# Kernel optimization log

Measured on AMD Instinct MI355X. Metric: run time of the kernel, lower is better.

The kernel has to match this reference:

```python
import jax, jax.numpy as jnp
import numpy as np

OUT_H, OUT_W = 7, 7
SPATIAL_SCALE = 0.0625


def setup_inputs() -> dict:
    key = jax.random.key(0)
    kf, kb, kx, ky, kw, kh = jax.random.split(key, 6)
    B, C, H, W = 2, 256, 38, 38
    n_rois = 64
    features = jax.random.normal(kf, (B, C, H, W), dtype=jnp.float32)
    bidx = jax.random.randint(kb, (n_rois,), 0, B)
    x1 = jax.random.randint(kx, (n_rois,), 0, 300)
    y1 = jax.random.randint(ky, (n_rois,), 0, 300)
    x2 = x1 + jax.random.randint(kw, (n_rois,), 32, 300)  # x2 < 600
    y2 = y1 + jax.random.randint(kh, (n_rois,), 32, 300)
    rois = jnp.stack([bidx, x1, y1, x2, y2], axis=1).astype(jnp.int32)
    return {"features": features, "rois": rois}


def _roi_max_pool(features, rois):
    # features: [B,C,H,W]; rois: [N,5] int (batch_idx,x1,y1,x2,y2) in image coords
    B, C, H, W = features.shape
    ridx = rois[:, 0]
    start_w = rois[:, 1].astype(jnp.float32) * SPATIAL_SCALE
    start_h = rois[:, 2].astype(jnp.float32) * SPATIAL_SCALE
    end_w = rois[:, 3].astype(jnp.float32) * SPATIAL_SCALE
    end_h = rois[:, 4].astype(jnp.float32) * SPATIAL_SCALE
    bin_h = jnp.maximum(end_h - start_h, 1.0) / OUT_H  # [N]
    bin_w = jnp.maximum(end_w - start_w, 1.0) / OUT_W

    oh = jnp.arange(OUT_H, dtype=jnp.float32)
    ow = jnp.arange(OUT_W, dtype=jnp.float32)
    # per-roi per-bin [start,end) extents, clipped to feature map (matches floor/ceil+clamp)
    hs = jnp.clip(jnp.floor(oh[None, :] * bin_h[:, None] + start_h[:, None]).astype(jnp.int32), 0, H)
    he = jnp.clip(jnp.ceil((oh[None, :] + 1.0) * bin_h[:, None] + start_h[:, None]).astype(jnp.int32), 0, H)
    ws = jnp.clip(jnp.floor(ow[None, :] * bin_w[:, None] + start_w[:, None]).astype(jnp.int32), 0, W)
    we = jnp.clip(jnp.ceil((ow[None, :] + 1.0) * bin_w[:, None] + start_w[:, None]).astype(jnp.int32), 0, W)

    hgrid = jnp.arange(H)
    wgrid = jnp.arange(W)
    mask_h = (hgrid[None, None, :] >= hs[:, :, None]) & (hgrid[None, None, :] < he[:, :, None])  # [N,oh,H]
    mask_w = (wgrid[None, None, :] >= ws[:, :, None]) & (wgrid[None, None, :] < we[:, :, None])  # [N,ow,W]

    feat = features[ridx]  # [N,C,H,W] gather per roi
    neg = jnp.float32(-jnp.inf)
    # separable masked max: first over W -> [N,C,H,ow]
    t = jnp.where(mask_w[:, None, None, :, :], feat[:, :, :, None, :], neg).max(axis=-1)
    # then over H -> [N,C,oh,ow]
    out = jnp.where(mask_h[:, None, :, :, None], t[:, :, None, :, :], neg).max(axis=3)
    # empty bins (h_end<=h_start or w_end<=w_start) stay zero in the original
    valid = mask_h.any(-1)[:, None, :, None] & mask_w.any(-1)[:, None, None, :]  # [N,1,oh,ow]
    return jnp.where(valid, out, jnp.float32(0.0))


def reference(features, rois):
    return _roi_max_pool(features, rois)
```

## Files before the change

kernel.cpp:

```cpp
#include <hip/hip_runtime.h>

#define OUT_HW 7
#define NCH    256
#define FH     38
#define FW     38


__global__ __launch_bounds__(256) void roi_pool_kernel(
    const float* __restrict__ feat,
    const int*   __restrict__ rois,
    float*       __restrict__ out,
    int total)
{
    int idx = blockIdx.x * blockDim.x + threadIdx.x;
    if (idx >= total) return;

    int ow = idx % OUT_HW;
    int oh = (idx / OUT_HW) % OUT_HW;
    int c  = (idx / (OUT_HW * OUT_HW)) % NCH;
    int r  = idx / (OUT_HW * OUT_HW * NCH);

    const int* roi = rois + r * 5;
    int ridx = roi[0];

    float sw = (float)roi[1] * 0.0625f;
    float sh = (float)roi[2] * 0.0625f;
    float ew = (float)roi[3] * 0.0625f;
    float eh = (float)roi[4] * 0.0625f;

    const float C7 = __uint_as_float(0x3E124925u);
    float bw = __fmul_rn(fmaxf(ew - sw, 1.0f), C7);
    float bh = __fmul_rn(fmaxf(eh - sh, 1.0f), C7);

    int hs = (int)floorf(fmaf((float)oh,       bh, sh));
    int he = (int)ceilf (fmaf((float)(oh + 1), bh, sh));
    int ws = (int)floorf(fmaf((float)ow,       bw, sw));
    int we = (int)ceilf (fmaf((float)(ow + 1), bw, sw));

    hs = min(max(hs, 0), FH);
    he = min(max(he, 0), FH);
    ws = min(max(ws, 0), FW);
    we = min(max(we, 0), FW);

    float m = 0.0f;
    if (hs < he && ws < we) {
        m = -INFINITY;
        const float* base = feat + ((size_t)ridx * NCH + c) * (FH * FW);
        for (int h = hs; h < he; ++h) {
            const float* row = base + h * FW;
            for (int w = ws; w < we; ++w) {
                m = fmaxf(m, row[w]);
            }
        }
    }
    out[idx] = m;
}

extern "C" void kernel_launch(void* const* d_in, const int* in_sizes, int n_in,
                              void* d_out, int out_size, void* d_ws, size_t ws_size,
                              hipStream_t stream) {
    const float* feat = (const float*)d_in[0];
    const int*   rois = (const int*)d_in[1];
    float*       out  = (float*)d_out;

    int total  = out_size;
    int blocks = (total + 255) / 256;
    roi_pool_kernel<<<blocks, 256, 0, stream>>>(feat, rois, out, total);
}
```

Measured before the change: 64.45 us.

## Stage each ROI channel plane in LDS with one wavefront per plane

Each wavefront now loads one whole 38x38 feature plane for its (roi, channel) pair into shared memory with coalesced float4 loads. Its first 49 lanes then compute the 7x7 bin maxima from LDS instead of issuing scattered global reads. This replaces many uncoalesced, partly redundant global loads with one contiguous plane copy, at the cost of loading the full plane even when the ROI covers only part of it. It also adds 23 KB of LDS per block and a block barrier.

```diff
diff --git a/kernel.cpp b/kernel.cpp
--- a/kernel.cpp
+++ b/kernel.cpp
@@ -4,24 +4,40 @@
 #define NCH    256
 #define FH     38
 #define FW     38
+#define PLANE  (FH * FW)
+#define PLANE4 (PLANE / 4)
+#define PLANE_PAD4 364
 
 
 __global__ __launch_bounds__(256) void roi_pool_kernel(
     const float* __restrict__ feat,
     const int*   __restrict__ rois,
-    float*       __restrict__ out,
-    int total)
+    float*       __restrict__ out)
 {
-    int idx = blockIdx.x * blockDim.x + threadIdx.x;
-    if (idx >= total) return;
+    __shared__ float4 lds4[4][PLANE_PAD4];
 
-    int ow = idx % OUT_HW;
-    int oh = (idx / OUT_HW) % OUT_HW;
-    int c  = (idx / (OUT_HW * OUT_HW)) % NCH;
-    int r  = idx / (OUT_HW * OUT_HW * NCH);
+    int tid  = threadIdx.x;
+    int wv   = tid >> 6;
+    int lane = tid & 63;
+    int p    = blockIdx.x * 4 + wv;
+    int c    = p & (NCH - 1);
+    int r    = p >> 8;
 
     const int* roi = rois + r * 5;
     int ridx = roi[0];
+
+    const float4* src4 = (const float4*)(feat + ((size_t)ridx * NCH + c) * PLANE);
+    float4* dst4 = &lds4[wv][0];
+    #pragma unroll
+    for (int i = 0; i < 6; ++i) {
+        int j = lane + i * 64;
+        if (j < PLANE4) dst4[j] = src4[j];
+    }
+    __syncthreads();
+
+    if (lane >= OUT_HW * OUT_HW) return;
+    int oh = lane / OUT_HW;
+    int ow = lane - oh * OUT_HW;
 
     float sw = (float)roi[1] * 0.0625f;
     float sh = (float)roi[2] * 0.0625f;
@@ -45,15 +61,15 @@
     float m = 0.0f;
     if (hs < he && ws < we) {
         m = -INFINITY;
-        const float* base = feat + ((size_t)ridx * NCH + c) * (FH * FW);
+        const float* pl = (const float*)&lds4[wv][0];
         for (int h = hs; h < he; ++h) {
-            const float* row = base + h * FW;
+            const float* row = pl + h * FW;
             for (int w = ws; w < we; ++w) {
                 m = fmaxf(m, row[w]);
             }
         }
     }
-    out[idx] = m;
+    out[(size_t)p * (OUT_HW * OUT_HW) + lane] = m;
 }
 
 extern "C" void kernel_launch(void* const* d_in, const int* in_sizes, int n_in,
@@ -63,7 +79,7 @@
     const int*   rois = (const int*)d_in[1];
     float*       out  = (float*)d_out;
 
-    int total  = out_size;
-    int blocks = (total + 255) / 256;
-    roi_pool_kernel<<<blocks, 256, 0, stream>>>(feat, rois, out, total);
+    int planes = out_size / (OUT_HW * OUT_HW);
+    int blocks = planes / 4;
+    roi_pool_kernel<<<blocks, 256, 0, stream>>>(feat, rois, out);
 }
```

Result: no change. 64.40 us (-0.1%).
